# Performance work log

Measured on AMD Instinct MI355X. Metric: run time of the kernel, lower is better.

Reference implementation:

```python
import jax, jax.numpy as jnp
import numpy as np

BN_EPS = 1e-5


def setup_inputs() -> dict:
    key = jax.random.key(0)
    ks = jax.random.split(key, 6)
    B, N, M, C1, C2 = 8, 8192, 2048, 128, 256
    in_ch = C1 + C2  # 384
    return {
        "xyz1": jax.random.uniform(ks[0], (B, N, 3), dtype=jnp.float32),
        "xyz2": jax.random.uniform(ks[1], (B, M, 3), dtype=jnp.float32),
        "features1": jax.random.normal(ks[2], (B, C1, N), dtype=jnp.float32),
        "features2": jax.random.normal(ks[3], (B, C2, M), dtype=jnp.float32),
        # Conv1d(kernel_size=1, bias=False) weights, squeezed to [out, in]
        "conv_w0": jax.random.normal(ks[4], (256, in_ch), dtype=jnp.float32) * 0.05,
        "gamma0": jnp.ones((256,), dtype=jnp.float32),
        "beta0": jnp.zeros((256,), dtype=jnp.float32),
        "conv_w1": jax.random.normal(ks[5], (256, 256), dtype=jnp.float32) * 0.05,
        "gamma1": jnp.ones((256,), dtype=jnp.float32),
        "beta1": jnp.zeros((256,), dtype=jnp.float32),
    }


def _conv_bn_relu(x, w, gamma, beta):
    # 1x1 Conv1d (no bias) == per-point channel matmul: [B,Cin,N] -> [B,Cout,N]
    x = jnp.einsum("oc,bcn->bon", w, x)
    # BatchNorm1d in training mode: batch stats over (B, N), biased variance
    mu = jnp.mean(x, axis=(0, 2), keepdims=True)
    var = jnp.var(x, axis=(0, 2), keepdims=True)
    x = (x - mu) * jax.lax.rsqrt(var + BN_EPS)
    x = x * gamma[None, :, None] + beta[None, :, None]
    return jax.nn.relu(x)


def reference(xyz1, xyz2, features1, features2,
              conv_w0, gamma0, beta0, conv_w1, gamma1, beta1):
    # squared pairwise distances [B, N, M] (broadcast diff reduced over coord dim)
    diff = xyz1[:, :, None, :] - xyz2[:, None, :, :]  # [B,N,M,3]
    dists = jnp.sum(diff * diff, axis=-1)             # [B,N,M]
    idx = jnp.argmin(dists, axis=-1)                  # [B,N] nearest downsampled point

    # per-batch gather: features2[b, :, idx[b]] -> [B, C2, N]
    interp = jax.vmap(lambda f, i: f[:, i])(features2, idx)

    x = jnp.concatenate([features1, interp], axis=1)  # [B, C1+C2, N]
    x = _conv_bn_relu(x, conv_w0, gamma0, beta0)
    x = _conv_bn_relu(x, conv_w1, gamma1, beta1)
    return x
```

## Files before the change

### kernel.cpp

```cpp
#include <hip/hip_runtime.h>
#include <stdint.h>

typedef unsigned short u16;
typedef unsigned int u32;
typedef __attribute__((ext_vector_type(8))) short short8;
typedef __attribute__((ext_vector_type(4))) float floatx4;

__device__ __forceinline__ u16 f2b(float f) {
  union { float f; u32 u; } c; c.f = f;
  u32 u = c.u;
  u += 0x7fffu + ((u >> 16) & 1u);
  return (u16)(u >> 16);
}
__device__ __forceinline__ float b2f(u16 h) {
  union { u32 u; float f; } c; c.u = ((u32)h) << 16;
  return c.f;
}

__global__ void cast_bf16_k(const float* __restrict__ in, u16* __restrict__ out, int n) {
  int i = blockIdx.x * 256 + threadIdx.x;
  if (i < n) out[i] = f2b(in[i]);
}

__global__ void transpose_cast_k(const float* __restrict__ in, u16* __restrict__ out, int C, int N) {
  __shared__ u16 tile[64][72];
  int b = blockIdx.z;
  int c0 = blockIdx.y * 64, n0 = blockIdx.x * 64;
  const float* src = in + ((size_t)b * C + c0) * N + n0;
  int t = threadIdx.x;
#pragma unroll
  for (int i = 0; i < 4; i++) {
    int id = t + i * 256;
    int c = id >> 4, nq = (id & 15) * 4;
    float4 v = *(const float4*)(src + (size_t)c * N + nq);
    tile[nq + 0][c] = f2b(v.x);
    tile[nq + 1][c] = f2b(v.y);
    tile[nq + 2][c] = f2b(v.z);
    tile[nq + 3][c] = f2b(v.w);
  }
  __syncthreads();
  int n = t >> 2, ch = (t & 3) * 16;
  u16* dst = out + ((size_t)b * N + n0 + n) * C + c0 + ch;
  uint4 a = *(const uint4*)&tile[n][ch];
  uint4 bb = *(const uint4*)&tile[n][ch + 8];
  *(uint4*)dst = a;
  *(uint4*)(dst + 8) = bb;
}

__global__ void argmin_part_k(const float* __restrict__ xyz1, const float* __restrict__ xyz2,
                              float2* __restrict__ cand) {
  __shared__ float4 s2[512];
  int b = blockIdx.z, mq = blockIdx.y, nq = blockIdx.x;
  const float* x2 = xyz2 + ((size_t)b * 2048 + mq * 512) * 3;
  for (int i = threadIdx.x; i < 512; i += 256)
    s2[i] = make_float4(x2[i * 3], x2[i * 3 + 1], x2[i * 3 + 2], 0.f);
  __syncthreads();
  int n = nq * 256 + threadIdx.x;
  const float* p1 = xyz1 + ((size_t)b * 8192 + n) * 3;
  float x = p1[0], y = p1[1], z = p1[2];
  float best = 3.0e38f; int bi = 0;
#pragma unroll 4
  for (int m = 0; m < 512; m++) {
    float4 q = s2[m];
    float dx = x - q.x, dy = y - q.y, dz = z - q.z;
    float d = dx * dx + dy * dy + dz * dz;
    if (d < best) { best = d; bi = m; }
  }
  cand[(size_t)mq * 65536 + (size_t)b * 8192 + n] = make_float2(best, __int_as_float(mq * 512 + bi));
}

__global__ void argmin_combine_k(const float2* __restrict__ cand, int* __restrict__ idx) {
  int p = blockIdx.x * 256 + threadIdx.x;
  float bd = 3.0e38f; int bi = 0;
#pragma unroll
  for (int q = 0; q < 4; q++) {
    float2 c = cand[(size_t)q * 65536 + p];
    if (c.x < bd) { bd = c.x; bi = __float_as_int(c.y); }
  }
  idx[p] = bi;
}

__global__ __launch_bounds__(256) void gemm1_k(const u16* __restrict__ w0b, const u16* __restrict__ f1t,
                                               const u16* __restrict__ f2t, const int* __restrict__ idx,
                                               u16* __restrict__ y0) {
  __shared__ u16 As[128 * 72];
  __shared__ u16 Bs[128 * 72];
  __shared__ int sidx[128];
  int t = threadIdx.x;
  int pt0 = blockIdx.x * 128;
  int o0 = blockIdx.y * 128;
  int b = pt0 >> 13;
  if (t < 128) sidx[t] = idx[pt0 + t];
  floatx4 zero = {0.f, 0.f, 0.f, 0.f};
  floatx4 acc[4][4];
#pragma unroll
  for (int i = 0; i < 4; i++)
#pragma unroll
    for (int j = 0; j < 4; j++) acc[i][j] = zero;
  int lane = t & 63, wave = t >> 6;
  int wrow = (wave >> 1) * 64, wcol = (wave & 1) * 64;
  int lr = lane & 15, lq = lane >> 4;

  for (int k0 = 0; k0 < 384; k0 += 64) {
    __syncthreads();
#pragma unroll
    for (int i = 0; i < 4; i++) {
      int id = t + i * 256;
      int row = id >> 3, ch = (id & 7) * 8;
      *(uint4*)&As[row * 72 + ch] = *(const uint4*)(w0b + (size_t)(o0 + row) * 384 + k0 + ch);
    }
    if (k0 < 128) {
#pragma unroll
      for (int i = 0; i < 4; i++) {
        int id = t + i * 256;
        int row = id >> 3, ch = (id & 7) * 8;
        *(uint4*)&Bs[row * 72 + ch] = *(const uint4*)(f1t + (size_t)(pt0 + row) * 128 + k0 + ch);
      }
    } else {
#pragma unroll
      for (int i = 0; i < 4; i++) {
        int id = t + i * 256;
        int row = id >> 3, ch = (id & 7) * 8;
        *(uint4*)&Bs[row * 72 + ch] =
            *(const uint4*)(f2t + ((size_t)(b << 11) + sidx[row]) * 256 + (k0 - 128) + ch);
      }
    }
    __syncthreads();
#pragma unroll
    for (int ks = 0; ks < 2; ks++) {
      int kk = ks * 32 + lq * 8;
      short8 af[4], bf[4];
#pragma unroll
      for (int i = 0; i < 4; i++) af[i] = *(const short8*)&As[(wrow + i * 16 + lr) * 72 + kk];
#pragma unroll
      for (int j = 0; j < 4; j++) bf[j] = *(const short8*)&Bs[(wcol + j * 16 + lr) * 72 + kk];
#pragma unroll
      for (int i = 0; i < 4; i++)
#pragma unroll
        for (int j = 0; j < 4; j++)
          acc[i][j] = __builtin_amdgcn_mfma_f32_16x16x32_bf16(af[i], bf[j], acc[i][j], 0, 0, 0);
    }
  }
#pragma unroll
  for (int i = 0; i < 4; i++) {
#pragma unroll
    for (int j = 0; j < 4; j++) {
      int o = o0 + wrow + i * 16 + lq * 4;
      int p = pt0 + wcol + j * 16 + lr;
      uint2 pk;
      pk.x = (u32)f2b(acc[i][j][0]) | ((u32)f2b(acc[i][j][1]) << 16);
      pk.y = (u32)f2b(acc[i][j][2]) | ((u32)f2b(acc[i][j][3]) << 16);
      *(uint2*)&y0[(size_t)p * 256 + o] = pk;
    }
  }
}

__global__ __launch_bounds__(256) void gemm2_k(const u16* __restrict__ w1b, const u16* __restrict__ y0,
                                               const float* __restrict__ scale0, const float* __restrict__ shift0,
                                               u16* __restrict__ y1) {
  __shared__ u16 As[128 * 72];
  __shared__ u16 Bs[128 * 72];
  __shared__ float ssc[256], ssh[256];
  int t = threadIdx.x;
  ssc[t] = scale0[t];
  ssh[t] = shift0[t];
  int pt0 = blockIdx.x * 128;
  int o0 = blockIdx.y * 128;
  floatx4 zero = {0.f, 0.f, 0.f, 0.f};
  floatx4 acc[4][4];
#pragma unroll
  for (int i = 0; i < 4; i++)
#pragma unroll
    for (int j = 0; j < 4; j++) acc[i][j] = zero;
  int lane = t & 63, wave = t >> 6;
  int wrow = (wave >> 1) * 64, wcol = (wave & 1) * 64;
  int lr = lane & 15, lq = lane >> 4;

  for (int k0 = 0; k0 < 256; k0 += 64) {
    __syncthreads();
#pragma unroll
    for (int i = 0; i < 4; i++) {
      int id = t + i * 256;
      int row = id >> 3, ch = (id & 7) * 8;
      *(uint4*)&As[row * 72 + ch] = *(const uint4*)(w1b + (size_t)(o0 + row) * 256 + k0 + ch);
    }
#pragma unroll
    for (int i = 0; i < 4; i++) {
      int id = t + i * 256;
      int row = id >> 3, ch = (id & 7) * 8;
      uint4 raw = *(const uint4*)(y0 + (size_t)(pt0 + row) * 256 + k0 + ch);
      u32 rw[4] = {raw.x, raw.y, raw.z, raw.w};
      u32 ow[4];
#pragma unroll
      for (int w = 0; w < 4; w++) {
        int k = k0 + ch + w * 2;
        float v0 = b2f((u16)(rw[w] & 0xffffu));
        float v1 = b2f((u16)(rw[w] >> 16));
        v0 = fmaxf(v0 * ssc[k] + ssh[k], 0.f);
        v1 = fmaxf(v1 * ssc[k + 1] + ssh[k + 1], 0.f);
        ow[w] = (u32)f2b(v0) | ((u32)f2b(v1) << 16);
      }
      uint4 ov; ov.x = ow[0]; ov.y = ow[1]; ov.z = ow[2]; ov.w = ow[3];
      *(uint4*)&Bs[row * 72 + ch] = ov;
    }
    __syncthreads();
#pragma unroll
    for (int ks = 0; ks < 2; ks++) {
      int kk = ks * 32 + lq * 8;
      short8 af[4], bf[4];
#pragma unroll
      for (int i = 0; i < 4; i++) af[i] = *(const short8*)&As[(wrow + i * 16 + lr) * 72 + kk];
#pragma unroll
      for (int j = 0; j < 4; j++) bf[j] = *(const short8*)&Bs[(wcol + j * 16 + lr) * 72 + kk];
#pragma unroll
      for (int i = 0; i < 4; i++)
#pragma unroll
        for (int j = 0; j < 4; j++)
          acc[i][j] = __builtin_amdgcn_mfma_f32_16x16x32_bf16(af[i], bf[j], acc[i][j], 0, 0, 0);
    }
  }
#pragma unroll
  for (int i = 0; i < 4; i++) {
#pragma unroll
    for (int j = 0; j < 4; j++) {
      int o = o0 + wrow + i * 16 + lq * 4;
      int p = pt0 + wcol + j * 16 + lr;
      uint2 pk;
      pk.x = (u32)f2b(acc[i][j][0]) | ((u32)f2b(acc[i][j][1]) << 16);
      pk.y = (u32)f2b(acc[i][j][2]) | ((u32)f2b(acc[i][j][3]) << 16);
      *(uint2*)&y1[(size_t)p * 256 + o] = pk;
    }
  }
}

__global__ void stats_k(const u16* __restrict__ y, float* __restrict__ sum, float* __restrict__ sq) {
  int o = threadIdx.x;
  const u16* base = y + (size_t)blockIdx.x * 65536 + o;
  float s = 0.f, q = 0.f;
  for (int p = 0; p < 256; p++) {
    float v = b2f(base[(size_t)p * 256]);
    s += v; q += v * v;
  }
  atomicAdd(&sum[o], s);
  atomicAdd(&sq[o], q);
}

__global__ void bnparam_k(const float* __restrict__ sum, const float* __restrict__ sq,
                          const float* __restrict__ gamma, const float* __restrict__ beta,
                          float* __restrict__ scale, float* __restrict__ shift) {
  int o = threadIdx.x;
  float mean = sum[o] * (1.f / 65536.f);
  float var = sq[o] * (1.f / 65536.f) - mean * mean;
  var = fmaxf(var, 0.f);
  float r = rsqrtf(var + 1e-5f);
  float sc = gamma[o] * r;
  scale[o] = sc;
  shift[o] = beta[o] - mean * sc;
}

__global__ void finalize_k(const u16* __restrict__ y1, const float* __restrict__ scale,
                           const float* __restrict__ shift, float* __restrict__ out) {
  __shared__ float tile[64][65];
  int b = blockIdx.z, o0 = blockIdx.y * 64, n0 = blockIdx.x * 64;
  int t = threadIdx.x;
  int pl = t >> 2, ch = (t & 3) * 16;
  const u16* src = y1 + ((size_t)(b * 8192 + n0 + pl)) * 256 + o0 + ch;
  uint4 r0 = *(const uint4*)src;
  uint4 r1 = *(const uint4*)(src + 8);
  u16 hv[16];
  *(uint4*)&hv[0] = r0;
  *(uint4*)&hv[8] = r1;
#pragma unroll
  for (int e = 0; e < 16; e++) {
    int o = o0 + ch + e;
    float v = b2f(hv[e]) * scale[o] + shift[o];
    tile[pl][ch + e] = fmaxf(v, 0.f);
  }
  __syncthreads();
  int ol = t >> 2, nch = (t & 3) * 16;
  float* dst = out + ((size_t)(b * 256 + o0 + ol)) * 8192 + n0 + nch;
#pragma unroll
  for (int j = 0; j < 16; j += 4) {
    float4 v = make_float4(tile[nch + j][ol], tile[nch + j + 1][ol],
                           tile[nch + j + 2][ol], tile[nch + j + 3][ol]);
    *(float4*)(dst + j) = v;
  }
}

extern "C" void kernel_launch(void* const* d_in, const int* in_sizes, int n_in,
                              void* d_out, int out_size, void* d_ws, size_t ws_size,
                              hipStream_t stream) {
  const float* xyz1      = (const float*)d_in[0];
  const float* xyz2      = (const float*)d_in[1];
  const float* features1 = (const float*)d_in[2];
  const float* features2 = (const float*)d_in[3];
  const float* conv_w0   = (const float*)d_in[4];
  const float* gamma0    = (const float*)d_in[5];
  const float* beta0     = (const float*)d_in[6];
  const float* conv_w1   = (const float*)d_in[7];
  const float* gamma1    = (const float*)d_in[8];
  const float* beta1     = (const float*)d_in[9];
  float* out = (float*)d_out;

  char* ws = (char*)d_ws;
  size_t off = 0;
  auto alloc = [&](size_t bytes) {
    char* p = ws + off;
    off = (off + bytes + 4095) & ~(size_t)4095;
    return p;
  };
  int*   idx    = (int*)alloc(65536 * 4);
  float* sums   = (float*)alloc(4 * 256 * 4);
  float* params = (float*)alloc(4 * 256 * 4);
  u16*   w0b    = (u16*)alloc(256 * 384 * 2);
  u16*   w1b    = (u16*)alloc(256 * 256 * 2);
  u16*   f1t    = (u16*)alloc((size_t)65536 * 128 * 2);
  u16*   f2t    = (u16*)alloc((size_t)16384 * 256 * 2);
  u16*   y0     = (u16*)alloc((size_t)65536 * 256 * 2);
  u16*   y1     = (u16*)alloc((size_t)65536 * 256 * 2);
  float2* cand  = (float2*)f1t;

  hipMemsetAsync(sums, 0, 4 * 256 * 4, stream);
  cast_bf16_k<<<dim3(384), 256, 0, stream>>>(conv_w0, w0b, 98304);
  cast_bf16_k<<<dim3(256), 256, 0, stream>>>(conv_w1, w1b, 65536);
  argmin_part_k<<<dim3(32, 4, 8), 256, 0, stream>>>(xyz1, xyz2, cand);
  argmin_combine_k<<<dim3(256), 256, 0, stream>>>(cand, idx);
  transpose_cast_k<<<dim3(128, 2, 8), 256, 0, stream>>>(features1, f1t, 128, 8192);
  transpose_cast_k<<<dim3(32, 4, 8), 256, 0, stream>>>(features2, f2t, 256, 2048);
  gemm1_k<<<dim3(512, 2), 256, 0, stream>>>(w0b, f1t, f2t, idx, y0);
  stats_k<<<dim3(256), 256, 0, stream>>>(y0, sums + 0, sums + 256);
  bnparam_k<<<1, 256, 0, stream>>>(sums + 0, sums + 256, gamma0, beta0, params + 0, params + 256);
  gemm2_k<<<dim3(512, 2), 256, 0, stream>>>(w1b, y0, params + 0, params + 256, y1);
  stats_k<<<dim3(256), 256, 0, stream>>>(y1, sums + 512, sums + 768);
  bnparam_k<<<1, 256, 0, stream>>>(sums + 512, sums + 768, gamma1, beta1, params + 512, params + 768);
  finalize_k<<<dim3(128, 4, 8), 256, 0, stream>>>(y1, params + 512, params + 768, out);
}
```

Measured before the change: 274.4 us.

## Use direct global-to-LDS loads with XOR swizzle in GEMMs; register-block argmin

The GEMM kernels now fill the A tile (and gemm1's B tile, including the gathered f2t rows) with global_load_lds 16-byte transfers into an XOR-swizzled unpadded LDS layout. This skips the register round trip and avoids bank conflicts on the fragment reads. The argmin kernel now processes four query points per thread over 256-point xyz2 chunks, giving 8 partial candidates that the combine kernel reduces. The aim is to cut LDS staging overhead and raise per-thread ALU reuse, but correctness depends on the swizzle mapping matching the wave-wide contiguous LDS write pattern of global_load_lds.

```diff
diff --git a/kernel.cpp b/kernel.cpp
--- a/kernel.cpp
+++ b/kernel.cpp
@@ -15,6 +15,11 @@
 __device__ __forceinline__ float b2f(u16 h) {
   union { u32 u; float f; } c; c.u = ((u32)h) << 16;
   return c.f;
+}
+
+__device__ __forceinline__ void glds16(const void* g, void* l) {
+  __builtin_amdgcn_global_load_lds((__attribute__((address_space(1))) void*)g,
+                                   (__attribute__((address_space(3))) void*)l, 16, 0, 0);
 }
 
 __global__ void cast_bf16_k(const float* __restrict__ in, u16* __restrict__ out, int n) {
@@ -49,31 +54,46 @@
 
 __global__ void argmin_part_k(const float* __restrict__ xyz1, const float* __restrict__ xyz2,
                               float2* __restrict__ cand) {
-  __shared__ float4 s2[512];
+  __shared__ float4 s2[256];
   int b = blockIdx.z, mq = blockIdx.y, nq = blockIdx.x;
-  const float* x2 = xyz2 + ((size_t)b * 2048 + mq * 512) * 3;
-  for (int i = threadIdx.x; i < 512; i += 256)
-    s2[i] = make_float4(x2[i * 3], x2[i * 3 + 1], x2[i * 3 + 2], 0.f);
-  __syncthreads();
-  int n = nq * 256 + threadIdx.x;
-  const float* p1 = xyz1 + ((size_t)b * 8192 + n) * 3;
-  float x = p1[0], y = p1[1], z = p1[2];
-  float best = 3.0e38f; int bi = 0;
+  const float* x2 = xyz2 + ((size_t)b * 2048 + mq * 256) * 3;
+  int t = threadIdx.x;
+  s2[t] = make_float4(x2[t * 3], x2[t * 3 + 1], x2[t * 3 + 2], 0.f);
+  __syncthreads();
+  int n0 = nq * 1024 + t;
+  float px[4], py[4], pz[4];
+#pragma unroll
+  for (int q = 0; q < 4; q++) {
+    const float* p1 = xyz1 + ((size_t)b * 8192 + n0 + q * 256) * 3;
+    px[q] = p1[0]; py[q] = p1[1]; pz[q] = p1[2];
+  }
+  float best[4] = {3.0e38f, 3.0e38f, 3.0e38f, 3.0e38f};
+  int bi[4] = {0, 0, 0, 0};
 #pragma unroll 4
-  for (int m = 0; m < 512; m++) {
-    float4 q = s2[m];
-    float dx = x - q.x, dy = y - q.y, dz = z - q.z;
-    float d = dx * dx + dy * dy + dz * dz;
-    if (d < best) { best = d; bi = m; }
-  }
-  cand[(size_t)mq * 65536 + (size_t)b * 8192 + n] = make_float2(best, __int_as_float(mq * 512 + bi));
+  for (int m = 0; m < 256; m++) {
+    float4 qq = s2[m];
+#pragma unroll
+    for (int q = 0; q < 4; q++) {
+      float dx = px[q] - qq.x, dy = py[q] - qq.y, dz = pz[q] - qq.z;
+      float d = fmaf(dz, dz, fmaf(dy, dy, dx * dx));
+      bool c = d < best[q];
+      best[q] = c ? d : best[q];
+      bi[q] = c ? m : bi[q];
+    }
+  }
+#pragma unroll
+  for (int q = 0; q < 4; q++) {
+    int n = n0 + q * 256;
+    cand[(size_t)mq * 65536 + (size_t)b * 8192 + n] =
+        make_float2(best[q], __int_as_float(mq * 256 + bi[q]));
+  }
 }
 
 __global__ void argmin_combine_k(const float2* __restrict__ cand, int* __restrict__ idx) {
   int p = blockIdx.x * 256 + threadIdx.x;
   float bd = 3.0e38f; int bi = 0;
 #pragma unroll
-  for (int q = 0; q < 4; q++) {
+  for (int q = 0; q < 8; q++) {
     float2 c = cand[(size_t)q * 65536 + p];
     if (c.x < bd) { bd = c.x; bi = __float_as_int(c.y); }
   }
@@ -83,12 +103,11 @@
 __global__ __launch_bounds__(256) void gemm1_k(const u16* __restrict__ w0b, const u16* __restrict__ f1t,
                                                const u16* __restrict__ f2t, const int* __restrict__ idx,
                                                u16* __restrict__ y0) {
-  __shared__ u16 As[128 * 72];
-  __shared__ u16 Bs[128 * 72];
+  __shared__ u16 As[128 * 64];
+  __shared__ u16 Bs[128 * 64];
   __shared__ int sidx[128];
   int t = threadIdx.x;
-  int pt0 = blockIdx.x * 128;
-  int o0 = blockIdx.y * 128;
+  int pt0 = blockIdx.x * 128, o0 = blockIdx.y * 128;
   int b = pt0 >> 13;
   if (t < 128) sidx[t] = idx[pt0 + t];
   floatx4 zero = {0.f, 0.f, 0.f, 0.f};
@@ -100,40 +119,45 @@
   int lane = t & 63, wave = t >> 6;
   int wrow = (wave >> 1) * 64, wcol = (wave & 1) * 64;
   int lr = lane & 15, lq = lane >> 4;
-
+  int srow = lane >> 3;
+  int sch = ((lane & 7) ^ srow) * 8;
+  __syncthreads();
+  int rowS[4], gidxB[4];
+#pragma unroll
+  for (int i = 0; i < 4; i++) {
+    rowS[i] = (i * 4 + wave) * 8 + srow;
+    gidxB[i] = sidx[rowS[i]];
+  }
+
+#pragma unroll
   for (int k0 = 0; k0 < 384; k0 += 64) {
     __syncthreads();
 #pragma unroll
-    for (int i = 0; i < 4; i++) {
-      int id = t + i * 256;
-      int row = id >> 3, ch = (id & 7) * 8;
-      *(uint4*)&As[row * 72 + ch] = *(const uint4*)(w0b + (size_t)(o0 + row) * 384 + k0 + ch);
-    }
+    for (int i = 0; i < 4; i++)
+      glds16(w0b + (size_t)(o0 + rowS[i]) * 384 + k0 + sch, &As[(i * 4 + wave) * 512]);
     if (k0 < 128) {
 #pragma unroll
+      for (int i = 0; i < 4; i++)
+        glds16(f1t + (size_t)(pt0 + rowS[i]) * 128 + k0 + sch, &Bs[(i * 4 + wave) * 512]);
+    } else {
+#pragma unroll
+      for (int i = 0; i < 4; i++)
+        glds16(f2t + ((size_t)(b << 11) + gidxB[i]) * 256 + (k0 - 128) + sch, &Bs[(i * 4 + wave) * 512]);
+    }
+    __syncthreads();
+#pragma unroll
+    for (int ks = 0; ks < 2; ks++) {
+      short8 af[4], bf[4];
+#pragma unroll
       for (int i = 0; i < 4; i++) {
-        int id = t + i * 256;
-        int row = id >> 3, ch = (id & 7) * 8;
-        *(uint4*)&Bs[row * 72 + ch] = *(const uint4*)(f1t + (size_t)(pt0 + row) * 128 + k0 + ch);
+        int row = wrow + i * 16 + lr;
+        af[i] = *(const short8*)&As[row * 64 + ((((ks << 2) | lq) ^ (lr & 7)) << 3)];
       }
-    } else {
-#pragma unroll
-      for (int i = 0; i < 4; i++) {
-        int id = t + i * 256;
-        int row = id >> 3, ch = (id & 7) * 8;
-        *(uint4*)&Bs[row * 72 + ch] =
-            *(const uint4*)(f2t + ((size_t)(b << 11) + sidx[row]) * 256 + (k0 - 128) + ch);
+#pragma unroll
+      for (int j = 0; j < 4; j++) {
+        int row = wcol + j * 16 + lr;
+        bf[j] = *(const short8*)&Bs[row * 64 + ((((ks << 2) | lq) ^ (lr & 7)) << 3)];
       }
-    }
-    __syncthreads();
-#pragma unroll
-    for (int ks = 0; ks < 2; ks++) {
-      int kk = ks * 32 + lq * 8;
-      short8 af[4], bf[4];
-#pragma unroll
-      for (int i = 0; i < 4; i++) af[i] = *(const short8*)&As[(wrow + i * 16 + lr) * 72 + kk];
-#pragma unroll
-      for (int j = 0; j < 4; j++) bf[j] = *(const short8*)&Bs[(wcol + j * 16 + lr) * 72 + kk];
 #pragma unroll
       for (int i = 0; i < 4; i++)
 #pragma unroll
@@ -158,14 +182,13 @@
 __global__ __launch_bounds__(256) void gemm2_k(const u16* __restrict__ w1b, const u16* __restrict__ y0,
                                                const float* __restrict__ scale0, const float* __restrict__ shift0,
                                                u16* __restrict__ y1) {
-  __shared__ u16 As[128 * 72];
+  __shared__ u16 As[128 * 64];
   __shared__ u16 Bs[128 * 72];
   __shared__ float ssc[256], ssh[256];
   int t = threadIdx.x;
   ssc[t] = scale0[t];
   ssh[t] = shift0[t];
-  int pt0 = blockIdx.x * 128;
-  int o0 = blockIdx.y * 128;
+  int pt0 = blockIdx.x * 128, o0 = blockIdx.y * 128;
   floatx4 zero = {0.f, 0.f, 0.f, 0.f};
   floatx4 acc[4][4];
 #pragma unroll
@@ -175,14 +198,17 @@
   int lane = t & 63, wave = t >> 6;
   int wrow = (wave >> 1) * 64, wcol = (wave & 1) * 64;
   int lr = lane & 15, lq = lane >> 4;
-
+  int srow = lane >> 3;
+  int sch = ((lane & 7) ^ srow) * 8;
+  __syncthreads();
+
+#pragma unroll
   for (int k0 = 0; k0 < 256; k0 += 64) {
     __syncthreads();
 #pragma unroll
     for (int i = 0; i < 4; i++) {
-      int id = t + i * 256;
-      int row = id >> 3, ch = (id & 7) * 8;
-      *(uint4*)&As[row * 72 + ch] = *(const uint4*)(w1b + (size_t)(o0 + row) * 256 + k0 + ch);
+      int rowA = (i * 4 + wave) * 8 + srow;
+      glds16(w1b + (size_t)(o0 + rowA) * 256 + k0 + sch, &As[(i * 4 + wave) * 512]);
     }
 #pragma unroll
     for (int i = 0; i < 4; i++) {
@@ -209,7 +235,10 @@
       int kk = ks * 32 + lq * 8;
       short8 af[4], bf[4];
 #pragma unroll
-      for (int i = 0; i < 4; i++) af[i] = *(const short8*)&As[(wrow + i * 16 + lr) * 72 + kk];
+      for (int i = 0; i < 4; i++) {
+        int row = wrow + i * 16 + lr;
+        af[i] = *(const short8*)&As[row * 64 + ((((ks << 2) | lq) ^ (lr & 7)) << 3)];
+      }
 #pragma unroll
       for (int j = 0; j < 4; j++) bf[j] = *(const short8*)&Bs[(wcol + j * 16 + lr) * 72 + kk];
 #pragma unroll
@@ -323,7 +352,7 @@
   hipMemsetAsync(sums, 0, 4 * 256 * 4, stream);
   cast_bf16_k<<<dim3(384), 256, 0, stream>>>(conv_w0, w0b, 98304);
   cast_bf16_k<<<dim3(256), 256, 0, stream>>>(conv_w1, w1b, 65536);
-  argmin_part_k<<<dim3(32, 4, 8), 256, 0, stream>>>(xyz1, xyz2, cand);
+  argmin_part_k<<<dim3(8, 8, 8), 256, 0, stream>>>(xyz1, xyz2, cand);
   argmin_combine_k<<<dim3(256), 256, 0, stream>>>(cand, idx);
   transpose_cast_k<<<dim3(128, 2, 8), 256, 0, stream>>>(features1, f1t, 128, 8192);
   transpose_cast_k<<<dim3(32, 4, 8), 256, 0, stream>>>(features2, f2t, 256, 2048);
```

Result: faster. 268.7 us (-2.1%).
